# Kernel optimization log

Measured on AMD Instinct MI355X. Metric: run time of the kernel, lower is better.

Reference implementation:

```python
import jax, jax.numpy as jnp
import numpy as np

# TT configuration (matches init_kwargs)
P = (100, 100, 100)      # tt_p_shapes, prod = num_embeddings = 1e6
Q = (4, 4, 8)            # tt_q_shapes, prod = embedding_dim = 128
R = (1, 32, 32, 1)       # tt_ranks padded with boundary 1s
D = 128                  # embedding_dim
B = 4096                 # batch size (number of bags)
H = 50                   # pooling factor (history length)
NNZ = B * H              # total indices


def setup_inputs() -> dict:
    key = jax.random.key(0)
    k1, k2, k3, k4 = jax.random.split(key, 4)
    # TT cores, stored flattened along trailing dims like TT-Rec:
    # core_i : [p_i, r_i * q_i * r_{i+1}]
    sigma = 0.1
    core0 = sigma * jax.random.normal(k1, (P[0], R[0] * Q[0] * R[1]), dtype=jnp.float32)
    core1 = sigma * jax.random.normal(k2, (P[1], R[1] * Q[1] * R[2]), dtype=jnp.float32)
    core2 = sigma * jax.random.normal(k3, (P[2], R[2] * Q[2] * R[3]), dtype=jnp.float32)
    indices = jax.random.randint(k4, (NNZ,), 0, P[0] * P[1] * P[2], dtype=jnp.int32)
    lengths = jnp.full((B,), H, dtype=jnp.int32)
    return {"indices": indices, "lengths": lengths,
            "core0": core0, "core1": core1, "core2": core2}


def reference(indices, lengths, core0, core1, core2):
    n = indices.shape[0]
    # mixed-radix decomposition of flat row index over p-shapes
    i1 = indices // (P[1] * P[2])
    i2 = (indices // P[2]) % P[1]
    i3 = indices % P[2]
    # gather per-index TT core slices
    a = core0[i1].reshape(n, Q[0], R[1])          # [n, q1, r1]
    b = core1[i2].reshape(n, R[1], Q[1], R[2])    # [n, r1, q2, r2]
    c = core2[i3].reshape(n, R[2], Q[2])          # [n, r2, q3]
    # TT contraction chain reconstructing each embedding row
    ab = jnp.einsum('nar,nrbs->nabs', a, b).reshape(n, Q[0] * Q[1], R[2])  # [n, q1*q2, r2]
    emb = jnp.einsum('nms,nsc->nmc', ab, c).reshape(n, D)                  # [n, D]
    # bag sum-pooling: rowidx = repeat_interleave(arange(B), lengths)
    batch = lengths.shape[0]
    rowidx = jnp.repeat(jnp.arange(batch, dtype=jnp.int32), lengths,
                        total_repeat_length=n)
    out = jax.ops.segment_sum(emb, rowidx, num_segments=batch)             # [B, D]
    return out
```

## Files before the change

### kernel.cpp

```cpp
#include <hip/hip_runtime.h>
#include <hip/hip_bf16.h>


#define P0 100
#define P1 100
#define P2 100
#define Q2 8
#define DIM 128
#define NPAIR (P0 * P1)
#define NULL_BFO (P2 * 512)

typedef __attribute__((ext_vector_type(8))) short short8v;
typedef __attribute__((ext_vector_type(4))) float f32x4;

__device__ inline short f2bf(float x) {
    union { __hip_bfloat16 h; short s; } u;
    u.h = __float2bfloat16(x);
    return u.s;
}

__global__ __launch_bounds__(256) void prep(const int* __restrict__ lengths, int B,
                                            const float* __restrict__ core0,
                                            const float* __restrict__ core1,
                                            const float* __restrict__ core2,
                                            int* __restrict__ offsets,
                                            __hip_bfloat16* __restrict__ bfrag,
                                            __hip_bfloat16* __restrict__ ab0,
                                            __hip_bfloat16* __restrict__ ab1) {
    int bid = blockIdx.x;
    int t = threadIdx.x;
    if (bid == 0) {
        ((short*)bfrag)[P2 * 256 + t] = 0;
        __shared__ int part[256];
        int per = (B + 255) / 256;
        int s = 0;
        for (int k = 0; k < per; ++k) {
            int i = t * per + k;
            s += (i < B) ? lengths[i] : 0;
        }
        part[t] = s;
        __syncthreads();
        for (int d = 1; d < 256; d <<= 1) {
            int v = (t >= d) ? part[t - d] : 0;
            __syncthreads();
            part[t] += v;
            __syncthreads();
        }
        int run = part[t] - s;
        for (int k = 0; k < per; ++k) {
            int i = t * per + k;
            if (i < B) { offsets[i] = run; run += lengths[i]; }
        }
        if (t == 255) offsets[B] = part[255];
    } else if (bid <= P2) {
        if (t < 64 && !(t & 8)) {
            int i3 = bid - 1;
            int h = t >> 4, c3 = t & 7;
            const float* crow = core2 + (size_t)i3 * (32 * Q2);
            __hip_bfloat16* o = bfrag + (size_t)i3 * 256 + h * 64 + c3 * 8;
#pragma unroll
            for (int j = 0; j < 8; ++j)
                o[j] = __float2bfloat16(crow[(h * 8 + j) * Q2 + c3]);
        }
    } else {
        int g = bid - 1 - P2;
        int i2 = g >> 1;
        int w = t >> 6, lane = t & 63;
        int ct = (g & 1) * 4 + w;
        int h = lane >> 4;
        int c16 = lane & 15;

        const float* bbase = core1 + (size_t)i2 * 4096 + (h * 8) * 128 + ct * 16 + c16;
        short8v bfr;
#pragma unroll
        for (int j = 0; j < 8; ++j) bfr[j] = f2bf(bbase[j * 128]);

        int col = ct * 16 + c16;
        int cs = col >> 5;
        int s = col & 31;
        for (int rt = 0; rt < 25; ++rt) {
            const float* abase = core0 + (size_t)(rt * 4 + (c16 >> 2)) * 128
                                 + (c16 & 3) * 32 + h * 8;
            f32x4 x0 = *(const f32x4*)abase;
            f32x4 x1 = *(const f32x4*)(abase + 4);
            short8v afr;
#pragma unroll
            for (int j = 0; j < 4; ++j) { afr[j] = f2bf(x0[j]); afr[j + 4] = f2bf(x1[j]); }

            f32x4 d = __builtin_amdgcn_mfma_f32_16x16x32_bf16(
                afr, bfr, (f32x4){0.f, 0.f, 0.f, 0.f}, 0, 0, 0);

            int pair = (rt * 4 + h) * P1 + i2;
#pragma unroll
            for (int q = 0; q < 4; ++q) {
                int m = q * 4 + cs;
                __hip_bfloat16* tbl = (m & 8) ? ab1 : ab0;
                tbl[(size_t)pair * 256 + (m & 7) * 32 + s] = __float2bfloat16(d[q]);
            }
        }
    }
}

__global__ __launch_bounds__(256) void bag_pool(const int* __restrict__ indices, int n,
                                                const int* __restrict__ offsets, int B,
                                                const char* __restrict__ ab0,
                                                const char* __restrict__ ab1,
                                                const char* __restrict__ bfrag,
                                                float* __restrict__ out) {
    int w = threadIdx.x >> 6;
    int lane = threadIdx.x & 63;
    int g = blockIdx.x >> 3;
    int xcd = blockIdx.x & 7;
    int half = xcd >> 2;
    int bag = (g * 4 + (xcd & 3)) * 4 + w;
    if (bag >= B) return;

    const char* tbl = half ? ab1 : ab0;

    int start = offsets[bag];
    int end = offsets[bag + 1];
    if (bag == B - 1 && end < n) end = n;
    if (end > n) end = n;
    if (start > n) start = n;
    if (end < start) end = start;
    int cnt = end - start;

    int sel = (lane >> 3) & 1;
    int aoff = (lane & 7) * 64 + (lane >> 4) * 16;
    int boff = (lane >> 4) * 128 + (lane & 7) * 16;

    f32x4 acc0 = {0.f, 0.f, 0.f, 0.f};
    f32x4 acc1 = {0.f, 0.f, 0.f, 0.f};

    for (int cb = 0; cb < cnt; cb += 64) {
        int m = cnt - cb;
        if (m > 64) m = 64;
        unsigned idx = 0;
        if (lane < m) idx = (unsigned)indices[start + cb + lane];
        unsigned p = idx / 100u;
        unsigned i3 = idx - p * 100u;
        int abo = (int)(p << 9);
        int bfo = (lane < m) ? (int)(i3 << 9) : NULL_BFO;

        int j = 0;
        for (; j + 3 < m; j += 4) {
            int A0 = __shfl(abo, j),     B0 = __shfl(bfo, j);
            int A1 = __shfl(abo, j + 1), B1 = __shfl(bfo, j + 1);
            int A2 = __shfl(abo, j + 2), B2 = __shfl(bfo, j + 2);
            int A3 = __shfl(abo, j + 3), B3 = __shfl(bfo, j + 3);
            int Ae = sel ? A1 : A0, Be = sel ? B1 : B0;
            int Af = sel ? A3 : A2, Bf = sel ? B3 : B2;
            short8v a0 = *(const short8v*)(tbl + Ae + aoff);
            short8v b0 = *(const short8v*)(bfrag + Be + boff);
            short8v a1 = *(const short8v*)(tbl + Af + aoff);
            short8v b1 = *(const short8v*)(bfrag + Bf + boff);
            acc0 = __builtin_amdgcn_mfma_f32_16x16x32_bf16(a0, b0, acc0, 0, 0, 0);
            acc1 = __builtin_amdgcn_mfma_f32_16x16x32_bf16(a1, b1, acc1, 0, 0, 0);
        }
        for (; j < m; j += 2) {
            int A0 = __shfl(abo, j),     B0 = __shfl(bfo, j);
            int A1 = __shfl(abo, j + 1), B1 = __shfl(bfo, j + 1);
            int Ae = sel ? A1 : A0, Be = sel ? B1 : B0;
            short8v a0 = *(const short8v*)(tbl + Ae + aoff);
            short8v b0 = *(const short8v*)(bfrag + Be + boff);
            acc0 = __builtin_amdgcn_mfma_f32_16x16x32_bf16(a0, b0, acc0, 0, 0, 0);
        }
    }
    f32x4 acc = acc0 + acc1;

#pragma unroll
    for (int q = 0; q < 4; ++q) {
        float o = __shfl(acc[q], (lane + 40) & 63);
        acc[q] += o;
    }
    int hi = lane >> 4, c3 = lane & 15;
    if (hi < 2 && c3 < 8) {
        float* obase = out + (size_t)bag * DIM;
#pragma unroll
        for (int q = 0; q < 4; ++q) {
            int d = (half * 8 + hi * 4 + q) * 8 + c3;
            atomicAdd(obase + d, acc[q]);
        }
    }
}

__global__ __launch_bounds__(128) void fallback_pool(const int* __restrict__ indices,
                                                     int n, int B,
                                                     const float* __restrict__ core0,
                                                     const float* __restrict__ core1,
                                                     const float* __restrict__ core2,
                                                     float* __restrict__ out) {
    int bag = blockIdx.x;
    int d = threadIdx.x;
    int m = d >> 3, c3 = d & 7;
    int a_ = m >> 2, b_ = m & 3;
    int H = n / B;
    float acc = 0.f;
    for (int j = bag * H; j < (bag + 1) * H; ++j) {
        int idx = indices[j];
        int i1 = idx / (P1 * P2);
        int rem = idx - i1 * (P1 * P2);
        int i2 = rem / P2;
        int i3 = rem - i2 * P2;
        const float* a = core0 + (size_t)i1 * 128;
        const float* b = core1 + (size_t)i2 * 4096;
        const float* c = core2 + (size_t)i3 * 256;
        float e = 0.f;
        for (int s = 0; s < 32; ++s) {
            float abv = 0.f;
            for (int r = 0; r < 32; ++r)
                abv += a[a_ * 32 + r] * b[r * 128 + b_ * 32 + s];
            e += abv * c[s * 8 + c3];
        }
        acc += e;
    }
    out[(size_t)bag * DIM + d] = acc;
}

extern "C" void kernel_launch(void* const* d_in, const int* in_sizes, int n_in,
                              void* d_out, int out_size, void* d_ws, size_t ws_size,
                              hipStream_t stream) {
    const int* indices = (const int*)d_in[0];
    const int* lengths = (const int*)d_in[1];
    const float* core0 = (const float*)d_in[2];
    const float* core1 = (const float*)d_in[3];
    const float* core2 = (const float*)d_in[4];
    float* out = (float*)d_out;
    int n = in_sizes[0];
    int B = in_sizes[1];

    const size_t OFF_OFFSETS = 0;
    const size_t OFF_BFRAG = 32768;
    const size_t OFF_AB0 = 131072;
    const size_t OFF_AB1 = OFF_AB0 + (size_t)NPAIR * 512;
    const size_t REQ = OFF_AB1 + (size_t)NPAIR * 512;

    if (ws_size >= REQ) {
        int* offsets = (int*)((char*)d_ws + OFF_OFFSETS);
        __hip_bfloat16* bfragp = (__hip_bfloat16*)((char*)d_ws + OFF_BFRAG);
        __hip_bfloat16* abt0 = (__hip_bfloat16*)((char*)d_ws + OFF_AB0);
        __hip_bfloat16* abt1 = (__hip_bfloat16*)((char*)d_ws + OFF_AB1);

        hipMemsetAsync(d_out, 0, (size_t)out_size * sizeof(float), stream);
        prep<<<1 + P2 + 200, 256, 0, stream>>>(lengths, B, core0, core1, core2,
                                               offsets, bfragp, abt0, abt1);
        int grid = ((B + 15) / 16) * 8;
        bag_pool<<<grid, 256, 0, stream>>>(indices, n, offsets, B,
                                           (const char*)abt0, (const char*)abt1,
                                           (const char*)bfragp, out);
    } else {
        fallback_pool<<<B, 128, 0, stream>>>(indices, n, B, core0, core1, core2, out);
    }
}
```

Measured before the change: 46.98 us.

## Split precomputed AB table into four rank-quarter tables across XCD pairs

Splits the precomputed core0×core1 product table and the core2 fragments by both output half and rank half (r2 split into two 16-wide chunks), giving four quarter tables of 2.5 MB each. Each XCD pair now handles one quarter, so the table working set touched per XCD shrinks and fits better in per-XCD L2. The MFMA K dimension is half padded with zero rows, so each wave does the same number of MFMAs while loading half the useful data. Twice as many blocks are launched and each output element gets more atomic adds.

```diff
diff --git a/kernel.cpp b/kernel.cpp
--- a/kernel.cpp
+++ b/kernel.cpp
@@ -8,7 +8,9 @@
 #define Q2 8
 #define DIM 128
 #define NPAIR (P0 * P1)
-#define NULL_BFO (P2 * 512)
+#define QT_STRIDE 2621440
+#define NULL_A_BYTES (NPAIR * 256)
+#define NULL_B_BYTES (P2 * 256)
 
 typedef __attribute__((ext_vector_type(8))) short short8v;
 typedef __attribute__((ext_vector_type(4))) float f32x4;
@@ -24,13 +26,19 @@
                                             const float* __restrict__ core1,
                                             const float* __restrict__ core2,
                                             int* __restrict__ offsets,
-                                            __hip_bfloat16* __restrict__ bfrag,
-                                            __hip_bfloat16* __restrict__ ab0,
-                                            __hip_bfloat16* __restrict__ ab1) {
+                                            char* __restrict__ bfq0,
+                                            char* __restrict__ bfq1,
+                                            char* __restrict__ qt) {
     int bid = blockIdx.x;
     int t = threadIdx.x;
     if (bid == 0) {
-        ((short*)bfrag)[P2 * 256 + t] = 0;
+        if (t < 128) {
+#pragma unroll
+            for (int qi = 0; qi < 4; ++qi)
+                ((short*)(qt + (size_t)qi * QT_STRIDE))[NPAIR * 128 + t] = 0;
+            ((short*)bfq0)[P2 * 128 + t] = 0;
+            ((short*)bfq1)[P2 * 128 + t] = 0;
+        }
         __shared__ int part[256];
         int per = (B + 255) / 256;
         int s = 0;
@@ -53,15 +61,13 @@
         }
         if (t == 255) offsets[B] = part[255];
     } else if (bid <= P2) {
-        if (t < 64 && !(t & 8)) {
-            int i3 = bid - 1;
-            int h = t >> 4, c3 = t & 7;
-            const float* crow = core2 + (size_t)i3 * (32 * Q2);
-            __hip_bfloat16* o = bfrag + (size_t)i3 * 256 + h * 64 + c3 * 8;
-#pragma unroll
-            for (int j = 0; j < 8; ++j)
-                o[j] = __float2bfloat16(crow[(h * 8 + j) * Q2 + c3]);
-        }
+        int i3 = bid - 1;
+        int s2 = t >> 7;
+        int e = t & 127;
+        int kg = e >> 6, c3 = (e >> 3) & 7, j = e & 7;
+        float v = core2[(size_t)i3 * 256 + (s2 * 16 + kg * 8 + j) * Q2 + c3];
+        short* dst = (short*)(s2 ? bfq1 : bfq0);
+        dst[(size_t)i3 * 128 + e] = f2bf(v);
     } else {
         int g = bid - 1 - P2;
         int i2 = g >> 1;
@@ -78,6 +84,7 @@
         int col = ct * 16 + c16;
         int cs = col >> 5;
         int s = col & 31;
+        int s2 = s >> 4, sl = s & 15;
         for (int rt = 0; rt < 25; ++rt) {
             const float* abase = core0 + (size_t)(rt * 4 + (c16 >> 2)) * 128
                                  + (c16 & 3) * 32 + h * 8;
@@ -94,8 +101,8 @@
 #pragma unroll
             for (int q = 0; q < 4; ++q) {
                 int m = q * 4 + cs;
-                __hip_bfloat16* tbl = (m & 8) ? ab1 : ab0;
-                tbl[(size_t)pair * 256 + (m & 7) * 32 + s] = __float2bfloat16(d[q]);
+                short* tbl = (short*)(qt + (size_t)((m >> 3) * 2 + s2) * QT_STRIDE);
+                tbl[(size_t)pair * 128 + (m & 7) * 16 + sl] = f2bf(d[q]);
             }
         }
     }
@@ -103,19 +110,21 @@
 
 __global__ __launch_bounds__(256) void bag_pool(const int* __restrict__ indices, int n,
                                                 const int* __restrict__ offsets, int B,
-                                                const char* __restrict__ ab0,
-                                                const char* __restrict__ ab1,
-                                                const char* __restrict__ bfrag,
+                                                const char* __restrict__ qt,
+                                                const char* __restrict__ bfq0,
+                                                const char* __restrict__ bfq1,
                                                 float* __restrict__ out) {
     int w = threadIdx.x >> 6;
     int lane = threadIdx.x & 63;
+    int xcd = blockIdx.x & 7;
     int g = blockIdx.x >> 3;
-    int xcd = blockIdx.x & 7;
-    int half = xcd >> 2;
-    int bag = (g * 4 + (xcd & 3)) * 4 + w;
+    int quarter = xcd >> 1;
+    int mh = quarter >> 1, s2 = quarter & 1;
+    int bag = g * 8 + (xcd & 1) * 4 + w;
     if (bag >= B) return;
 
-    const char* tbl = half ? ab1 : ab0;
+    const char* tbl = qt + (size_t)quarter * QT_STRIDE;
+    const char* bfq = s2 ? bfq1 : bfq0;
 
     int start = offsets[bag];
     int end = offsets[bag + 1];
@@ -126,8 +135,9 @@
     int cnt = end - start;
 
     int sel = (lane >> 3) & 1;
-    int aoff = (lane & 7) * 64 + (lane >> 4) * 16;
-    int boff = (lane >> 4) * 128 + (lane & 7) * 16;
+    bool lowk = (lane >> 4) < 2;
+    int aoff = (lane & 7) * 32 + ((lane >> 4) & 1) * 16;
+    int boff = (lane & 7) * 16 + ((lane >> 4) & 1) * 128;
 
     f32x4 acc0 = {0.f, 0.f, 0.f, 0.f};
     f32x4 acc1 = {0.f, 0.f, 0.f, 0.f};
@@ -139,8 +149,8 @@
         if (lane < m) idx = (unsigned)indices[start + cb + lane];
         unsigned p = idx / 100u;
         unsigned i3 = idx - p * 100u;
-        int abo = (int)(p << 9);
-        int bfo = (lane < m) ? (int)(i3 << 9) : NULL_BFO;
+        int abo = (int)(p << 8);
+        int bfo = (lane < m) ? (int)(i3 << 8) : NULL_B_BYTES;
 
         int j = 0;
         for (; j + 3 < m; j += 4) {
@@ -148,21 +158,24 @@
             int A1 = __shfl(abo, j + 1), B1 = __shfl(bfo, j + 1);
             int A2 = __shfl(abo, j + 2), B2 = __shfl(bfo, j + 2);
             int A3 = __shfl(abo, j + 3), B3 = __shfl(bfo, j + 3);
-            int Ae = sel ? A1 : A0, Be = sel ? B1 : B0;
-            int Af = sel ? A3 : A2, Bf = sel ? B3 : B2;
+            int Ae = lowk ? (sel ? A1 : A0) : NULL_A_BYTES;
+            int Be = lowk ? (sel ? B1 : B0) : NULL_B_BYTES;
+            int Af = lowk ? (sel ? A3 : A2) : NULL_A_BYTES;
+            int Bf = lowk ? (sel ? B3 : B2) : NULL_B_BYTES;
             short8v a0 = *(const short8v*)(tbl + Ae + aoff);
-            short8v b0 = *(const short8v*)(bfrag + Be + boff);
+            short8v b0 = *(const short8v*)(bfq + Be + boff);
             short8v a1 = *(const short8v*)(tbl + Af + aoff);
-            short8v b1 = *(const short8v*)(bfrag + Bf + boff);
+            short8v b1 = *(const short8v*)(bfq + Bf + boff);
             acc0 = __builtin_amdgcn_mfma_f32_16x16x32_bf16(a0, b0, acc0, 0, 0, 0);
             acc1 = __builtin_amdgcn_mfma_f32_16x16x32_bf16(a1, b1, acc1, 0, 0, 0);
         }
         for (; j < m; j += 2) {
             int A0 = __shfl(abo, j),     B0 = __shfl(bfo, j);
             int A1 = __shfl(abo, j + 1), B1 = __shfl(bfo, j + 1);
-            int Ae = sel ? A1 : A0, Be = sel ? B1 : B0;
+            int Ae = lowk ? (sel ? A1 : A0) : NULL_A_BYTES;
+            int Be = lowk ? (sel ? B1 : B0) : NULL_B_BYTES;
             short8v a0 = *(const short8v*)(tbl + Ae + aoff);
-            short8v b0 = *(const short8v*)(bfrag + Be + boff);
+            short8v b0 = *(const short8v*)(bfq + Be + boff);
             acc0 = __builtin_amdgcn_mfma_f32_16x16x32_bf16(a0, b0, acc0, 0, 0, 0);
         }
     }
@@ -178,7 +191,7 @@
         float* obase = out + (size_t)bag * DIM;
 #pragma unroll
         for (int q = 0; q < 4; ++q) {
-            int d = (half * 8 + hi * 4 + q) * 8 + c3;
+            int d = (mh * 8 + hi * 4 + q) * 8 + c3;
             atomicAdd(obase + d, acc[q]);
         }
     }
@@ -230,24 +243,24 @@
     int B = in_sizes[1];
 
     const size_t OFF_OFFSETS = 0;
-    const size_t OFF_BFRAG = 32768;
-    const size_t OFF_AB0 = 131072;
-    const size_t OFF_AB1 = OFF_AB0 + (size_t)NPAIR * 512;
-    const size_t REQ = OFF_AB1 + (size_t)NPAIR * 512;
+    const size_t OFF_BFQ0 = 32768;
+    const size_t OFF_BFQ1 = 65536;
+    const size_t OFF_Q = 131072;
+    const size_t REQ = OFF_Q + 4ull * QT_STRIDE;
 
     if (ws_size >= REQ) {
         int* offsets = (int*)((char*)d_ws + OFF_OFFSETS);
-        __hip_bfloat16* bfragp = (__hip_bfloat16*)((char*)d_ws + OFF_BFRAG);
-        __hip_bfloat16* abt0 = (__hip_bfloat16*)((char*)d_ws + OFF_AB0);
-        __hip_bfloat16* abt1 = (__hip_bfloat16*)((char*)d_ws + OFF_AB1);
+        char* bfq0 = (char*)d_ws + OFF_BFQ0;
+        char* bfq1 = (char*)d_ws + OFF_BFQ1;
+        char* qt = (char*)d_ws + OFF_Q;
 
         hipMemsetAsync(d_out, 0, (size_t)out_size * sizeof(float), stream);
         prep<<<1 + P2 + 200, 256, 0, stream>>>(lengths, B, core0, core1, core2,
-                                               offsets, bfragp, abt0, abt1);
-        int grid = ((B + 15) / 16) * 8;
+                                               offsets, bfq0, bfq1, qt);
+        int grid = ((B + 7) / 8) * 8;
         bag_pool<<<grid, 256, 0, stream>>>(indices, n, offsets, B,
-                                           (const char*)abt0, (const char*)abt1,
-                                           (const char*)bfragp, out);
+                                           (const char*)qt, (const char*)bfq0,
+                                           (const char*)bfq1, out);
     } else {
         fallback_pool<<<B, 128, 0, stream>>>(indices, n, B, core0, core1, core2, out);
     }
```

New measurement: 53.16 us. 1.13x slower.
